# Kernel tuning notes

Hardware: AMD Instinct MI355X
Metric: run time of the kernel (lower is better)

Reference implementation:

```python
import jax, jax.numpy as jnp
import numpy as np

B, C, K, D = 2048, 100, 8, 64


def setup_inputs() -> dict:
    key = jax.random.key(0)
    k1, k2, k3, k4 = jax.random.split(key, 4)
    representation = jax.random.normal(k1, (B, D), dtype=jnp.float32)
    mixture_logits = 0.1 * jax.random.normal(k2, (C, K), dtype=jnp.float32)
    loc = jax.random.normal(k3, (C, K, D), dtype=jnp.float32)
    # lower-triangular with unit diagonal, small off-diagonal (matches 'random'/'zeros' init style)
    raw = 0.05 * jax.random.normal(k4, (C, K, D, D), dtype=jnp.float32)
    scale_tril = jnp.tril(raw, k=-1) + jnp.eye(D, dtype=jnp.float32)
    return {"representation": representation, "mixture_logits": mixture_logits,
            "loc": loc, "scale_tril": scale_tril}


def reference(representation, mixture_logits, loc, scale_tril):
    # representation: [B, D]; mixture_logits: [C, K]; loc: [C, K, D]; scale_tril: [C, K, D, D]
    d = representation.shape[-1]
    log2pi = jnp.log(jnp.asarray(2.0 * np.pi, dtype=representation.dtype))
    # residuals: [B, C, K, D] -> move batch last for batched triangular solve: [C, K, D, B]
    diff = representation[:, None, None, :] - loc[None]
    b = jnp.moveaxis(diff, 0, -1)
    # whiten: solve L z = (x - mu) for each (class, component)
    z = jax.lax.linalg.triangular_solve(scale_tril, b, left_side=True, lower=True)  # [C, K, D, B]
    quad = jnp.sum(z * z, axis=2)  # [C, K, B]
    # log|det Sigma|^{1/2} = sum log |diag(L)|
    logdet = jnp.sum(jnp.log(jnp.abs(jnp.diagonal(scale_tril, axis1=-2, axis2=-1))), axis=-1)  # [C, K]
    comp_lp = -0.5 * (quad + d * log2pi) - logdet[..., None]  # [C, K, B]
    mix = jax.nn.log_softmax(mixture_logits, axis=-1)  # [C, K]
    class_lp = jax.scipy.special.logsumexp(comp_lp + mix[..., None], axis=1)  # [C, B]
    logits = jax.nn.log_softmax(class_lp.T, axis=1)  # [B, C]
    return logits
```

## Files before the change

### kernel.cpp

```cpp
#include <hip/hip_runtime.h>
#include <math.h>

#define C_ 100
#define K_ 8
#define D_ 64
#define B_ 2048

using f16x8 = __attribute__((ext_vector_type(8))) _Float16;
using f32x4 = __attribute__((ext_vector_type(4))) float;

template <int CTRL>
__device__ __forceinline__ float dpp_xadd(float x) {
    int v = __builtin_amdgcn_update_dpp(0, __float_as_int(x), CTRL, 0xf, 0xf, true);
    return x + __int_as_float(v);
}
__device__ __forceinline__ float sum16(float x) {
    x = dpp_xadd<0xB1>(x);
    x = dpp_xadd<0x4E>(x);
    x = dpp_xadd<0x141>(x);
    x = dpp_xadd<0x140>(x);
    return x;
}

#define LS_S 68
#define AT_S 65
__global__ __launch_bounds__(64) void k_invert(const float* __restrict__ L_g,
                                               const float* __restrict__ rep,
                                               const float* __restrict__ loc_g,
                                               f16x8* __restrict__ ATf,
                                               _Float16* __restrict__ Xh,
                                               float* __restrict__ v_g,
                                               float* __restrict__ ld_g) {
    const int ck = blockIdx.x;
    const int j = threadIdx.x;
    __shared__ float Ls[D_][LS_S];
    __shared__ float At[D_][AT_S];
    __shared__ float mus[D_];

    for (int idx = ck * 64 + j; idx < B_ * D_; idx += C_ * K_ * 64)
        Xh[idx] = (_Float16)rep[idx];

    const float* Lsrc = L_g + (size_t)ck * D_ * D_;
#pragma unroll
    for (int t = 0; t < D_; ++t)
        Ls[t][j] = Lsrc[t * D_ + j];
    mus[j] = loc_g[ck * D_ + j];
    __syncthreads();

    {
        float ll = __logf(fabsf(Ls[j][j]));
        ll = sum16(ll);
        ll += __shfl_xor(ll, 16, 64);
        ll += __shfl_xor(ll, 32, 64);
        if (j == 0) ld_g[ck] = ll;
    }

    float a[D_];
    const float r0 = __builtin_amdgcn_rcpf(Ls[j][j]);
#pragma unroll
    for (int m = 0; m < D_; ++m) a[m] = (j == m) ? r0 : 0.f;

#pragma unroll
    for (int i = 1; i < D_; ++i) {
        float a0 = 0.f, a1 = 0.f, a2 = 0.f, a3 = 0.f;
#pragma unroll
        for (int m0 = 0; m0 + 3 < i; m0 += 4) {
            const float4 L4 = *reinterpret_cast<const float4*>(&Ls[i][m0]);
            a0 = fmaf(L4.x, a[m0 + 0], a0);
            a1 = fmaf(L4.y, a[m0 + 1], a1);
            a2 = fmaf(L4.z, a[m0 + 2], a2);
            a3 = fmaf(L4.w, a[m0 + 3], a3);
        }
#pragma unroll
        for (int m = i & ~3; m < i; ++m) a0 = fmaf(Ls[i][m], a[m], a0);
        const float acc = (a0 + a1) + (a2 + a3);
        const float nv = -acc * __builtin_amdgcn_rcpf(Ls[i][i]);
        a[i] = (j < i) ? nv : a[i];
    }

#pragma unroll
    for (int m = 0; m < D_; ++m) At[m][j] = a[m];
    __syncthreads();

    const int q8 = (j >> 4) * 8, cl = j & 15;
    float vpart[4];
#pragma unroll
    for (int dt = 0; dt < 4; ++dt) {
        vpart[dt] = 0.f;
#pragma unroll
        for (int ks = 0; ks < 2; ++ks) {
            f16x8 t;
#pragma unroll
            for (int s = 0; s < 8; ++s) {
                const _Float16 h = (_Float16)At[dt * 16 + cl][ks * 32 + q8 + s];
                t[s] = h;
                vpart[dt] = fmaf((float)h, mus[ks * 32 + q8 + s], vpart[dt]);
            }
            ATf[(size_t)ck * 512 + (dt * 2 + ks) * 64 + j] = t;
        }
        vpart[dt] += __shfl_xor(vpart[dt], 16, 64);
        vpart[dt] += __shfl_xor(vpart[dt], 32, 64);
    }
    if (j < 16) {
#pragma unroll
        for (int dt = 0; dt < 4; ++dt)
            v_g[(size_t)ck * D_ + dt * 16 + j] = vpart[dt];
    }
}

__global__ __launch_bounds__(512, 4) void k_main(const _Float16* __restrict__ Xh,
                                                 const f16x8* __restrict__ ATf,
                                                 const float* __restrict__ v_g,
                                                 const float* __restrict__ ml,
                                                 const float* __restrict__ ld_g,
                                                 float* __restrict__ clp_g) {
    const int c = blockIdx.y;
    const int b0 = blockIdx.x * 256;
    const int tid = threadIdx.x;
    const int wave = tid >> 6;
    const int lane = tid & 63;
    const int col = lane & 15;
    const int quad = lane >> 4;
    const int bw = b0 + wave * 32;

    __shared__ f16x8 Bs[K_ * 512];
    __shared__ float vs_s[K_ * D_];
    __shared__ float offs_s[K_];

    const f16x8* Bsrc = ATf + (size_t)c * K_ * 512;
#pragma unroll
    for (int k = 0; k < K_; ++k)
        Bs[k * 512 + tid] = Bsrc[k * 512 + tid];
    vs_s[tid] = v_g[(size_t)c * K_ * D_ + tid];
    if (tid < K_) {
        float vals[K_];
        float mx = -INFINITY;
#pragma unroll
        for (int k = 0; k < K_; ++k) { vals[k] = ml[c * K_ + k]; mx = fmaxf(mx, vals[k]); }
        float s = 0.f;
#pragma unroll
        for (int k = 0; k < K_; ++k) s += __expf(vals[k] - mx);
        const float lse = mx + __logf(s);
        offs_s[tid] = vals[tid] - lse - 58.8120661251f - ld_g[c * K_ + tid];
    }

    f16x8 Xf[2][2];
#pragma unroll
    for (int bt = 0; bt < 2; ++bt)
#pragma unroll
        for (int ks = 0; ks < 2; ++ks)
            Xf[bt][ks] = *reinterpret_cast<const f16x8*>(
                Xh + (size_t)(bw + bt * 16 + col) * D_ + ks * 32 + quad * 8);

    float m_run[2][4], s_run[2][4];
#pragma unroll
    for (int bt = 0; bt < 2; ++bt)
#pragma unroll
        for (int r = 0; r < 4; ++r) { m_run[bt][r] = -INFINITY; s_run[bt][r] = 0.f; }

    const f32x4 zero = {0.f, 0.f, 0.f, 0.f};
    __syncthreads();

    for (int k = 0; k < K_; ++k) {
        float vv[4];
#pragma unroll
        for (int dt = 0; dt < 4; ++dt)
            vv[dt] = vs_s[k * D_ + dt * 16 + col];
        const float offk = offs_s[k];

        f32x4 acc[2][4];
#pragma unroll
        for (int dt = 0; dt < 4; ++dt) {
            const f16x8 B0 = Bs[k * 512 + (dt * 2 + 0) * 64 + lane];
            const f16x8 B1 = Bs[k * 512 + (dt * 2 + 1) * 64 + lane];
#pragma unroll
            for (int bt = 0; bt < 2; ++bt) {
                acc[bt][dt] = __builtin_amdgcn_mfma_f32_16x16x32_f16(
                    Xf[bt][0], B0, zero, 0, 0, 0);
                acc[bt][dt] = __builtin_amdgcn_mfma_f32_16x16x32_f16(
                    Xf[bt][1], B1, acc[bt][dt], 0, 0, 0);
            }
        }

#pragma unroll
        for (int bt = 0; bt < 2; ++bt) {
            float p[4];
#pragma unroll
            for (int r = 0; r < 4; ++r) {
                float s = 0.f;
#pragma unroll
                for (int dt = 0; dt < 4; ++dt) {
                    const float z = acc[bt][dt][r] - vv[dt];
                    s = fmaf(z, z, s);
                }
                p[r] = s;
            }
#pragma unroll
            for (int r = 0; r < 4; ++r) p[r] = sum16(p[r]);
#pragma unroll
            for (int r = 0; r < 4; ++r) {
                const float lp = fmaf(-0.5f, p[r], offk);
                const float nm = fmaxf(m_run[bt][r], lp);
                s_run[bt][r] = s_run[bt][r] * __expf(m_run[bt][r] - nm) + __expf(lp - nm);
                m_run[bt][r] = nm;
            }
        }
    }

    if (col == 0) {
#pragma unroll
        for (int bt = 0; bt < 2; ++bt)
#pragma unroll
            for (int r = 0; r < 4; ++r) {
                const int b = bw + bt * 16 + quad * 4 + r;
                clp_g[(size_t)b * C_ + c] = m_run[bt][r] + __logf(s_run[bt][r]);
            }
    }
}

__global__ __launch_bounds__(256) void k_final(const float* __restrict__ clp,
                                               float* __restrict__ out) {
    const int wave = threadIdx.x >> 6;
    const int lane = threadIdx.x & 63;
    const int b = blockIdx.x * 4 + wave;
    const float* row = clp + (size_t)b * C_;
    const float x0 = row[lane];
    const float x1 = (lane < C_ - 64) ? row[64 + lane] : -INFINITY;
    float m = fmaxf(x0, x1);
    for (int o = 32; o > 0; o >>= 1) m = fmaxf(m, __shfl_xor(m, o, 64));
    float s = __expf(x0 - m) + ((lane < C_ - 64) ? __expf(x1 - m) : 0.f);
    for (int o = 32; o > 0; o >>= 1) s += __shfl_xor(s, o, 64);
    const float L = m + __logf(s);
    out[(size_t)b * C_ + lane] = x0 - L;
    if (lane < C_ - 64) out[(size_t)b * C_ + 64 + lane] = x1 - L;
}

extern "C" void kernel_launch(void* const* d_in, const int* in_sizes, int n_in,
                              void* d_out, int out_size, void* d_ws, size_t ws_size,
                              hipStream_t stream) {
    const float* rep = (const float*)d_in[0];
    const float* ml  = (const float*)d_in[1];
    const float* loc = (const float*)d_in[2];
    const float* st  = (const float*)d_in[3];
    float* out = (float*)d_out;

    char* w = (char*)d_ws;
    f16x8*    ATf = (f16x8*)w;
    _Float16* Xh  = (_Float16*)(w + 6553600);
    float*    v   = (float*)(w + 6815744);
    float*    ld  = (float*)(w + 7020544);
    float*    clp = (float*)(w + 7023744);

    k_invert<<<dim3(C_ * K_), dim3(64), 0, stream>>>(st, rep, loc, ATf, Xh, v, ld);
    k_main<<<dim3(B_ / 256, C_), dim3(512), 0, stream>>>(Xh, ATf, v, ml, ld, clp);
    k_final<<<dim3(B_ / 4), dim3(256), 0, stream>>>(clp, out);
}
```

Baseline: 119.3 us.

## Assign one mixture component per wave with register-resident B fragments

k_main now gives each of the 8 waves one mixture component, holding its whitening matrix fragments and offset vector in registers, and iterates over 8 batch sub-tiles loaded from a swizzled shared-memory X tile. Per-component quadratic forms go to shared memory and a final pass does the logsumexp over components. The class log-prob buffer becomes class-major so writes are coalesced, and k_final reads it strided. The intent is to stop restaging B tiles from LDS for every component and to cut the serial online-softmax. The cost is higher register pressure, an extra barrier, and uncoalesced strided reads in k_final.

```diff
diff --git a/kernel.cpp b/kernel.cpp
--- a/kernel.cpp
+++ b/kernel.cpp
@@ -24,13 +24,13 @@
 
 #define LS_S 68
 #define AT_S 65
-__global__ __launch_bounds__(64) void k_invert(const float* __restrict__ L_g,
-                                               const float* __restrict__ rep,
-                                               const float* __restrict__ loc_g,
-                                               f16x8* __restrict__ ATf,
-                                               _Float16* __restrict__ Xh,
-                                               float* __restrict__ v_g,
-                                               float* __restrict__ ld_g) {
+__global__ __launch_bounds__(64, 1) void k_invert(const float* __restrict__ L_g,
+                                                  const float* __restrict__ rep,
+                                                  const float* __restrict__ loc_g,
+                                                  f16x8* __restrict__ ATf,
+                                                  _Float16* __restrict__ Xh,
+                                                  float* __restrict__ v_g,
+                                                  float* __restrict__ ld_g) {
     const int ck = blockIdx.x;
     const int j = threadIdx.x;
     __shared__ float Ls[D_][LS_S];
@@ -117,21 +117,25 @@
     const int c = blockIdx.y;
     const int b0 = blockIdx.x * 256;
     const int tid = threadIdx.x;
-    const int wave = tid >> 6;
+    const int w = tid >> 6;
     const int lane = tid & 63;
     const int col = lane & 15;
     const int quad = lane >> 4;
-    const int bw = b0 + wave * 32;
-
-    __shared__ f16x8 Bs[K_ * 512];
-    __shared__ float vs_s[K_ * D_];
+
+    __shared__ f16x8 Xs[2048];
+    __shared__ float qk[K_][260];
     __shared__ float offs_s[K_];
 
-    const f16x8* Bsrc = ATf + (size_t)c * K_ * 512;
-#pragma unroll
-    for (int k = 0; k < K_; ++k)
-        Bs[k * 512 + tid] = Bsrc[k * 512 + tid];
-    vs_s[tid] = v_g[(size_t)c * K_ * D_ + tid];
+    const int ck = c * K_ + w;
+    f16x8 Bf[8];
+#pragma unroll
+    for (int f = 0; f < 8; ++f)
+        Bf[f] = ATf[(size_t)ck * 512 + f * 64 + lane];
+    float vv[4];
+#pragma unroll
+    for (int dt = 0; dt < 4; ++dt)
+        vv[dt] = v_g[(size_t)ck * D_ + dt * 16 + col];
+
     if (tid < K_) {
         float vals[K_];
         float mx = -INFINITY;
@@ -144,77 +148,75 @@
         offs_s[tid] = vals[tid] - lse - 58.8120661251f - ld_g[c * K_ + tid];
     }
 
-    f16x8 Xf[2][2];
-#pragma unroll
-    for (int bt = 0; bt < 2; ++bt)
-#pragma unroll
-        for (int ks = 0; ks < 2; ++ks)
-            Xf[bt][ks] = *reinterpret_cast<const f16x8*>(
-                Xh + (size_t)(bw + bt * 16 + col) * D_ + ks * 32 + quad * 8);
-
-    float m_run[2][4], s_run[2][4];
-#pragma unroll
-    for (int bt = 0; bt < 2; ++bt)
-#pragma unroll
-        for (int r = 0; r < 4; ++r) { m_run[bt][r] = -INFINITY; s_run[bt][r] = 0.f; }
+#pragma unroll
+    for (int p = 0; p < 4; ++p) {
+        const int u = p * 512 + tid;
+        const int q = u & 7, row = u >> 3;
+        const f16x8 val = *reinterpret_cast<const f16x8*>(
+            Xh + (size_t)(b0 + row) * D_ + q * 8);
+        const int s = row >> 5, bt = (row >> 4) & 1, cc = row & 15;
+        Xs[((s * 2 + bt) * 8 + q) * 16 + (q ^ cc)] = val;
+    }
+    __syncthreads();
 
     const f32x4 zero = {0.f, 0.f, 0.f, 0.f};
-    __syncthreads();
-
-    for (int k = 0; k < K_; ++k) {
-        float vv[4];
-#pragma unroll
-        for (int dt = 0; dt < 4; ++dt)
-            vv[dt] = vs_s[k * D_ + dt * 16 + col];
-        const float offk = offs_s[k];
+
+    for (int s = 0; s < 8; ++s) {
+        f16x8 Xf[2][2];
+#pragma unroll
+        for (int bt = 0; bt < 2; ++bt)
+#pragma unroll
+            for (int ks = 0; ks < 2; ++ks) {
+                const int q = ks * 4 + quad;
+                Xf[bt][ks] = Xs[((s * 2 + bt) * 8 + q) * 16 + (q ^ col)];
+            }
 
         f32x4 acc[2][4];
 #pragma unroll
-        for (int dt = 0; dt < 4; ++dt) {
-            const f16x8 B0 = Bs[k * 512 + (dt * 2 + 0) * 64 + lane];
-            const f16x8 B1 = Bs[k * 512 + (dt * 2 + 1) * 64 + lane];
-#pragma unroll
-            for (int bt = 0; bt < 2; ++bt) {
+        for (int bt = 0; bt < 2; ++bt)
+#pragma unroll
+            for (int dt = 0; dt < 4; ++dt) {
                 acc[bt][dt] = __builtin_amdgcn_mfma_f32_16x16x32_f16(
-                    Xf[bt][0], B0, zero, 0, 0, 0);
+                    Xf[bt][0], Bf[dt * 2 + 0], zero, 0, 0, 0);
                 acc[bt][dt] = __builtin_amdgcn_mfma_f32_16x16x32_f16(
-                    Xf[bt][1], B1, acc[bt][dt], 0, 0, 0);
-            }
-        }
+                    Xf[bt][1], Bf[dt * 2 + 1], acc[bt][dt], 0, 0, 0);
+            }
 
 #pragma unroll
         for (int bt = 0; bt < 2; ++bt) {
             float p[4];
 #pragma unroll
             for (int r = 0; r < 4; ++r) {
-                float s = 0.f;
+                float sum = 0.f;
 #pragma unroll
                 for (int dt = 0; dt < 4; ++dt) {
                     const float z = acc[bt][dt][r] - vv[dt];
-                    s = fmaf(z, z, s);
+                    sum = fmaf(z, z, sum);
                 }
-                p[r] = s;
+                p[r] = sum;
             }
 #pragma unroll
             for (int r = 0; r < 4; ++r) p[r] = sum16(p[r]);
-#pragma unroll
-            for (int r = 0; r < 4; ++r) {
-                const float lp = fmaf(-0.5f, p[r], offk);
-                const float nm = fmaxf(m_run[bt][r], lp);
-                s_run[bt][r] = s_run[bt][r] * __expf(m_run[bt][r] - nm) + __expf(lp - nm);
-                m_run[bt][r] = nm;
-            }
-        }
-    }
-
-    if (col == 0) {
-#pragma unroll
-        for (int bt = 0; bt < 2; ++bt)
-#pragma unroll
-            for (int r = 0; r < 4; ++r) {
-                const int b = bw + bt * 16 + quad * 4 + r;
-                clp_g[(size_t)b * C_ + c] = m_run[bt][r] + __logf(s_run[bt][r]);
-            }
+            if (col == 0) {
+                f32x4 pv = {p[0], p[1], p[2], p[3]};
+                *reinterpret_cast<f32x4*>(&qk[w][s * 32 + bt * 16 + quad * 4]) = pv;
+            }
+        }
+    }
+    __syncthreads();
+
+    if (tid < 256) {
+        float lp[K_];
+        float m = -INFINITY;
+#pragma unroll
+        for (int k = 0; k < K_; ++k) {
+            lp[k] = fmaf(-0.5f, qk[k][tid], offs_s[k]);
+            m = fmaxf(m, lp[k]);
+        }
+        float s = 0.f;
+#pragma unroll
+        for (int k = 0; k < K_; ++k) s += __expf(lp[k] - m);
+        clp_g[(size_t)c * B_ + b0 + tid] = m + __logf(s);
     }
 }
 
@@ -223,9 +225,8 @@
     const int wave = threadIdx.x >> 6;
     const int lane = threadIdx.x & 63;
     const int b = blockIdx.x * 4 + wave;
-    const float* row = clp + (size_t)b * C_;
-    const float x0 = row[lane];
-    const float x1 = (lane < C_ - 64) ? row[64 + lane] : -INFINITY;
+    const float x0 = clp[(size_t)lane * B_ + b];
+    const float x1 = (lane < C_ - 64) ? clp[(size_t)(64 + lane) * B_ + b] : -INFINITY;
     float m = fmaxf(x0, x1);
     for (int o = 32; o > 0; o >>= 1) m = fmaxf(m, __shfl_xor(m, o, 64));
     float s = __expf(x0 - m) + ((lane < C_ - 64) ? __expf(x1 - m) : 0.f);
```

New measurement: 112.4 us. 1.06x faster.
